# Kernel optimization log

Hardware: AMD Instinct MI355X
Metric: run time of the kernel (lower is better)

The kernel has to match this reference:

```python
import jax, jax.numpy as jnp
import numpy as np

B, S, D = 32, 2048, 64
SQRT_DIM = float(np.sqrt(D))  # scale=True -> divide by sqrt(dim)


def setup_inputs() -> dict:
    key = jax.random.key(0)
    kq, kk, kv, km = jax.random.split(key, 4)
    query = jax.random.normal(kq, (B, S, D), dtype=jnp.float32)
    key_t = jax.random.normal(kk, (B, S, D), dtype=jnp.float32)
    value = jax.random.normal(kv, (B, S, D), dtype=jnp.float32)
    mask = jax.random.randint(km, (B, S, S), 0, 2).astype(jnp.bool_)
    return {"query": query, "key": key_t, "value": value, "mask": mask}


def reference(query, key, value, mask):
    # score = Q @ K^T / sqrt(dim)   -> [B, S, S]
    score = jnp.einsum('bqd,bkd->bqk', query, key) / SQRT_DIM
    score = jnp.where(mask, jnp.float32(-1e9), score)  # masked_fill_
    attn = jax.nn.softmax(score, axis=-1)
    # context = attn @ V   -> [B, S, D]  (block_mask is None -> no gamma)
    context = jnp.einsum('bqk,bkd->bqd', attn, value)
    return (context, attn)
```

## Files before the change

kernel.cpp:

```cpp
#include <hip/hip_runtime.h>
#include <hip/hip_bf16.h>

#define BB 32
#define SS 2048
#define DD 64
#define NTH 256
#define QT 16
#define KTL 128
#define SCALE 0.125f

typedef __attribute__((ext_vector_type(4))) float f32x4;
typedef __attribute__((ext_vector_type(8))) short bf16x8;

union B8 { bf16x8 v; unsigned int u[4]; };

__device__ __forceinline__ unsigned int pk2bf(float a, float b) {
    __hip_bfloat162 h = __float22bfloat162_rn(make_float2(a, b));
    unsigned int u;
    __builtin_memcpy(&u, &h, 4);
    return u;
}
__device__ __forceinline__ float bf_lo(unsigned int w) {
    return __builtin_bit_cast(float, w << 16);
}
__device__ __forceinline__ float bf_hi(unsigned int w) {
    return __builtin_bit_cast(float, w & 0xffff0000u);
}

__global__ __launch_bounds__(NTH) void prepK(const float* __restrict__ K,
                                             unsigned short* __restrict__ Kbf) {
    const size_t i = (size_t)blockIdx.x * NTH + threadIdx.x;
    const float4* s = (const float4*)K;
    const float4 a = s[2 * i], c = s[2 * i + 1];
    uint4 w;
    w.x = pk2bf(a.x, a.y); w.y = pk2bf(a.z, a.w);
    w.z = pk2bf(c.x, c.y); w.w = pk2bf(c.z, c.w);
    ((uint4*)Kbf)[i] = w;
}

#define VPADF 68
__global__ __launch_bounds__(NTH) void prepV(const float* __restrict__ V,
                                             unsigned short* __restrict__ VTh,
                                             unsigned short* __restrict__ VTl) {
    __shared__ __align__(16) float lt[KTL * VPADF];
    const int t  = threadIdx.x;
    const int b  = blockIdx.x >> 4;
    const int ck = blockIdx.x & 15;
    const float4* Vs = (const float4*)(V + ((size_t)b * SS + ck * KTL) * DD);
    #pragma unroll
    for (int i = 0; i < 8; ++i) {
        const int f4 = i * NTH + t;
        float4 v = Vs[f4];
        const int kc = f4 >> 4, d4 = f4 & 15;
        *(float4*)&lt[kc * VPADF + d4 * 4] = v;
    }
    __syncthreads();
    const int d = t >> 2, kseg = t & 3;
    unsigned short* oh = VTh + ((size_t)b * DD + d) * SS + ck * KTL + kseg * 32;
    unsigned short* ol = VTl + ((size_t)b * DD + d) * SS + ck * KTL + kseg * 32;
    #pragma unroll
    for (int cch = 0; cch < 4; ++cch) {
        uint4 wh, wl;
        unsigned int* ph = (unsigned int*)&wh;
        unsigned int* pl = (unsigned int*)&wl;
        #pragma unroll
        for (int p = 0; p < 4; ++p) {
            const int k0 = kseg * 32 + cch * 8 + p * 2;
            const float a = lt[k0 * VPADF + d], c = lt[(k0 + 1) * VPADF + d];
            const unsigned int hw = pk2bf(a, c);
            ph[p] = hw;
            pl[p] = pk2bf(a - bf_lo(hw), c - bf_hi(hw));
        }
        *(uint4*)(oh + cch * 8) = wh;
        *(uint4*)(ol + cch * 8) = wl;
    }
}

__global__ __launch_bounds__(NTH, 4) void sdpa_mfma2(
    const float* __restrict__ Q, const int* __restrict__ M,
    const unsigned short* __restrict__ Kbf,
    const unsigned short* __restrict__ VTh, const unsigned short* __restrict__ VTl,
    float* __restrict__ ctx, float* __restrict__ attn)
{
    __shared__ __align__(16) unsigned char smem[17408];
    __shared__ float wsum[4][QT];
    __shared__ float inv_l[QT];
    unsigned short* bnc = (unsigned short*)smem;
    float*          scr = (float*)smem;

    const int t    = threadIdx.x;
    const int wave = t >> 6, l = t & 63, g = l >> 4, li = l & 15;
    const int b    = blockIdx.x >> 7;
    const int q0   = (blockIdx.x & 127) * QT;

    const unsigned short* Kb  = Kbf + (size_t)b * SS * DD;
    const unsigned short* Vhb = VTh + (size_t)b * DD * SS;
    const unsigned short* Vlb = VTl + (size_t)b * DD * SS;
    const int*   Mb   = M + ((size_t)b * SS + q0) * SS;
    float*       attb = attn + ((size_t)b * SS + q0) * SS;

    B8 qh[2], ql[2];
    {
        const float* qp = Q + ((size_t)(b * SS + q0 + li)) * DD + g * 8;
        #pragma unroll
        for (int h = 0; h < 2; ++h) {
            float f[8];
            *(float4*)&f[0] = *(const float4*)(qp + h * 32);
            *(float4*)&f[4] = *(const float4*)(qp + h * 32 + 4);
            #pragma unroll
            for (int i = 0; i < 4; ++i) {
                unsigned int hw = pk2bf(f[2*i], f[2*i+1]);
                qh[h].u[i] = hw;
                ql[h].u[i] = pk2bf(f[2*i] - bf_lo(hw), f[2*i+1] - bf_hi(hw));
            }
        }
    }

    const unsigned short* kf0 = Kb + (size_t)(wave * 32 + li) * DD + g * 8;

    auto qk = [&](int tl, f32x4& s0, f32x4& s1) {
        const unsigned short* p0 = kf0 + (size_t)tl * KTL * DD;
        #pragma unroll
        for (int h = 0; h < 2; ++h) {
            B8 k0, k1;
            k0.v = *(const bf16x8*)(p0 + 32 * h);
            k1.v = *(const bf16x8*)(p0 + 16 * DD + 32 * h);
            s0 = __builtin_amdgcn_mfma_f32_16x16x32_bf16(qh[h].v, k0.v, s0, 0, 0, 0);
            s0 = __builtin_amdgcn_mfma_f32_16x16x32_bf16(ql[h].v, k0.v, s0, 0, 0, 0);
            s1 = __builtin_amdgcn_mfma_f32_16x16x32_bf16(qh[h].v, k1.v, s1, 0, 0, 0);
            s1 = __builtin_amdgcn_mfma_f32_16x16x32_bf16(ql[h].v, k1.v, s1, 0, 0, 0);
        }
    };

    float lsum[4] = {0.f, 0.f, 0.f, 0.f};
    unsigned int mb0 = 0, mb1 = 0, mb2 = 0, mb3 = 0;

    #pragma unroll 1
    for (int tl = 0; tl < 16; ++tl) {
        const int kg0 = tl * KTL + wave * 32 + li;
        int m0a[4], m1a[4];
        #pragma unroll
        for (int r = 0; r < 4; ++r) {
            const size_t mo = (size_t)(g * 4 + r) * SS + kg0;
            m0a[r] = __builtin_nontemporal_load(&Mb[mo]);
            m1a[r] = __builtin_nontemporal_load(&Mb[mo + 16]);
        }
        f32x4 s0 = {0.f,0.f,0.f,0.f}, s1 = {0.f,0.f,0.f,0.f};
        qk(tl, s0, s1);
        unsigned int fl = 0;
        #pragma unroll
        for (int r = 0; r < 4; ++r) {
            float e0 = __expf(s0[r] * SCALE);
            float e1 = __expf(s1[r] * SCALE);
            if (m0a[r]) { fl |= 1u << r;       e0 = 0.f; }
            if (m1a[r]) { fl |= 1u << (4 + r); e1 = 0.f; }
            lsum[r] += e0 + e1;
        }
        mb0 = (mb0 >> 8) | (mb1 << 24);
        mb1 = (mb1 >> 8) | (mb2 << 24);
        mb2 = (mb2 >> 8) | (mb3 << 24);
        mb3 = (mb3 >> 8) | (fl << 24);
    }

    #pragma unroll
    for (int off = 8; off >= 1; off >>= 1)
        #pragma unroll
        for (int r = 0; r < 4; ++r)
            lsum[r] += __shfl_xor(lsum[r], off, 64);
    if (li == 0) {
        #pragma unroll
        for (int r = 0; r < 4; ++r) wsum[wave][g * 4 + r] = lsum[r];
    }
    __syncthreads();
    if (t < QT) inv_l[t] = 1.0f / (wsum[0][t] + wsum[1][t] + wsum[2][t] + wsum[3][t]);
    __syncthreads();
    float invl[4];
    #pragma unroll
    for (int r = 0; r < 4; ++r) invl[r] = inv_l[g * 4 + r];

    f32x4 cacc[4] = {{0.f,0.f,0.f,0.f},{0.f,0.f,0.f,0.f},{0.f,0.f,0.f,0.f},{0.f,0.f,0.f,0.f}};
    unsigned short* bw = bnc + wave * 512;

    #pragma unroll 1
    for (int tl = 0; tl < 16; ++tl) {
        f32x4 s0 = {0.f,0.f,0.f,0.f}, s1 = {0.f,0.f,0.f,0.f};
        qk(tl, s0, s1);
        const unsigned int fl = mb0 & 0xffu;
        mb0 = (mb0 >> 8) | (mb1 << 24);
        mb1 = (mb1 >> 8) | (mb2 << 24);
        mb2 = (mb2 >> 8) | (mb3 << 24);
        mb3 >>= 8;
        const int kg0 = tl * KTL + wave * 32 + li;
        #pragma unroll
        for (int r = 0; r < 4; ++r) {
            float e0 = ((fl >> r)       & 1u) ? 0.f : __expf(s0[r] * SCALE);
            float e1 = ((fl >> (4 + r)) & 1u) ? 0.f : __expf(s1[r] * SCALE);
            const size_t ao = (size_t)(g * 4 + r) * SS + kg0;
            attb[ao]      = e0 * invl[r];
            attb[ao + 16] = e1 * invl[r];
            const int q = g * 4 + r;
            const int b0 = li >> 3, b1 = (li + 16) >> 3;
            bw[((b0 * 16 + (q ^ b0)) << 3) + (li & 7)] = (unsigned short)pk2bf(e0, 0.f);
            bw[((b1 * 16 + (q ^ b1)) << 3) + (li & 7)] = (unsigned short)pk2bf(e1, 0.f);
        }
        B8 pf;
        pf.v = *(const bf16x8*)(bw + ((g * 16 + (li ^ g)) << 3));
        const size_t vcol = (size_t)tl * KTL + wave * 32 + g * 8;
        #pragma unroll
        for (int c = 0; c < 4; ++c) {
            const size_t voff = (size_t)(c * 16 + li) * SS + vcol;
            B8 vh, vl;
            vh.v = *(const bf16x8*)(Vhb + voff);
            vl.v = *(const bf16x8*)(Vlb + voff);
            cacc[c] = __builtin_amdgcn_mfma_f32_16x16x32_bf16(pf.v, vh.v, cacc[c], 0, 0, 0);
            cacc[c] = __builtin_amdgcn_mfma_f32_16x16x32_bf16(pf.v, vl.v, cacc[c], 0, 0, 0);
        }
    }

    __syncthreads();
    {
        const int row = wave * 64 + l;
        #pragma unroll
        for (int c = 0; c < 4; ++c)
            #pragma unroll
            for (int r = 0; r < 4; ++r)
                scr[row * 17 + c * 4 + r] = cacc[c][r];
    }
    __syncthreads();
    {
        const int q = t >> 4, d0 = (t & 15) * 4;
        float4 o;
        float* op = &o.x;
        #pragma unroll
        for (int dd = 0; dd < 4; ++dd) {
            const int d    = d0 + dd;
            const int lane = (q >> 2) * 16 + (d & 15);
            const int idx  = lane * 17 + (d >> 4) * 4 + (q & 3);
            float s = 0.f;
            #pragma unroll
            for (int w = 0; w < 4; ++w) s += scr[w * 64 * 17 + idx];
            op[dd] = s * inv_l[q];
        }
        *(float4*)(ctx + ((size_t)(b * SS + q0 + q)) * DD + d0) = o;
    }
}

extern "C" void kernel_launch(void* const* d_in, const int* in_sizes, int n_in,
                              void* d_out, int out_size, void* d_ws, size_t ws_size,
                              hipStream_t stream) {
    const float* Q = (const float*)d_in[0];
    const float* K = (const float*)d_in[1];
    const float* V = (const float*)d_in[2];
    const int*   M = (const int*)d_in[3];
    float* ctx  = (float*)d_out;
    float* attn = (float*)d_out + (size_t)BB * SS * DD;

    const size_t NE = (size_t)BB * SS * DD;
    unsigned short* Kbf = (unsigned short*)d_ws;
    unsigned short* VTh = Kbf + NE;
    unsigned short* VTl = VTh + NE;

    prepK<<<dim3((unsigned)(NE / 8 / NTH)), dim3(NTH), 0, stream>>>(K, Kbf);
    prepV<<<dim3(BB * (SS / KTL)), dim3(NTH), 0, stream>>>(V, VTh, VTl);
    sdpa_mfma2<<<dim3(BB * (SS / QT)), dim3(NTH), 0, stream>>>(Q, M, Kbf, VTh, VTl, ctx, attn);
}
```

Measured before the change: 1.287 ms.

## Prepack mask into bitmasks in separate kernel, raise occupancy, swizzle block order

Adds a packM kernel that compresses each row's int32 mask into per-lane 32-bit bitmasks, so the attention kernel loads four words per thread instead of streaming int mask values inside its first pass. The first pass drops the mask loads and the shift-register bookkeeping. It also raises launch bounds to 8 blocks per CU and swizzles the block index so neighbouring blocks spread across batches. The mask is still read in full once, but by a separate pass with an extra launch and workspace, and the higher occupancy target may force register spills.

```diff
diff --git a/kernel.cpp b/kernel.cpp
--- a/kernel.cpp
+++ b/kernel.cpp
@@ -76,8 +76,25 @@
     }
 }
 
-__global__ __launch_bounds__(NTH, 4) void sdpa_mfma2(
-    const float* __restrict__ Q, const int* __restrict__ M,
+__global__ __launch_bounds__(NTH) void packM(const int* __restrict__ M,
+                                             unsigned int* __restrict__ Mp) {
+    const int t = threadIdx.x, w = t >> 6, l = t & 63;
+    const size_t row = (size_t)blockIdx.x * 4 + w;
+    const int* mr = M + row * SS;
+    const int kb = (l >> 4) * 32 + (l & 15);
+    unsigned int bits = 0;
+    #pragma unroll
+    for (int tl = 0; tl < 16; ++tl) {
+        const int m0 = __builtin_nontemporal_load(&mr[tl * 128 + kb]);
+        const int m1 = __builtin_nontemporal_load(&mr[tl * 128 + kb + 16]);
+        bits |= (m0 ? 1u : 0u) << (2 * tl);
+        bits |= (m1 ? 1u : 0u) << (2 * tl + 1);
+    }
+    Mp[row * 64 + l] = bits;
+}
+
+__global__ __launch_bounds__(NTH, 8) void sdpa_mfma2(
+    const float* __restrict__ Q, const unsigned int* __restrict__ Mp,
     const unsigned short* __restrict__ Kbf,
     const unsigned short* __restrict__ VTh, const unsigned short* __restrict__ VTl,
     float* __restrict__ ctx, float* __restrict__ attn)
@@ -90,14 +107,22 @@
 
     const int t    = threadIdx.x;
     const int wave = t >> 6, l = t & 63, g = l >> 4, li = l & 15;
-    const int b    = blockIdx.x >> 7;
-    const int q0   = (blockIdx.x & 127) * QT;
+    const unsigned int bid = blockIdx.x;
+    const unsigned int swz = (bid & 7) * 512 + (bid >> 3);
+    const int b    = swz >> 7;
+    const int q0   = (swz & 127) * QT;
 
     const unsigned short* Kb  = Kbf + (size_t)b * SS * DD;
     const unsigned short* Vhb = VTh + (size_t)b * DD * SS;
     const unsigned short* Vlb = VTl + (size_t)b * DD * SS;
-    const int*   Mb   = M + ((size_t)b * SS + q0) * SS;
-    float*       attb = attn + ((size_t)b * SS + q0) * SS;
+    float* attb = attn + ((size_t)b * SS + q0) * SS;
+
+    unsigned int mreg[4];
+    {
+        const unsigned int* Mpb = Mp + ((size_t)b * SS + q0) * 64 + (wave * 16 + li);
+        #pragma unroll
+        for (int r = 0; r < 4; ++r) mreg[r] = Mpb[(size_t)(g * 4 + r) * 64];
+    }
 
     B8 qh[2], ql[2];
     {
@@ -133,68 +158,47 @@
     };
 
     float lsum[4] = {0.f, 0.f, 0.f, 0.f};
-    unsigned int mb0 = 0, mb1 = 0, mb2 = 0, mb3 = 0;
-
-    #pragma unroll 1
-    for (int tl = 0; tl < 16; ++tl) {
-        const int kg0 = tl * KTL + wave * 32 + li;
-        int m0a[4], m1a[4];
-        #pragma unroll
-        for (int r = 0; r < 4; ++r) {
-            const size_t mo = (size_t)(g * 4 + r) * SS + kg0;
-            m0a[r] = __builtin_nontemporal_load(&Mb[mo]);
-            m1a[r] = __builtin_nontemporal_load(&Mb[mo + 16]);
-        }
-        f32x4 s0 = {0.f,0.f,0.f,0.f}, s1 = {0.f,0.f,0.f,0.f};
-        qk(tl, s0, s1);
-        unsigned int fl = 0;
-        #pragma unroll
-        for (int r = 0; r < 4; ++r) {
-            float e0 = __expf(s0[r] * SCALE);
-            float e1 = __expf(s1[r] * SCALE);
-            if (m0a[r]) { fl |= 1u << r;       e0 = 0.f; }
-            if (m1a[r]) { fl |= 1u << (4 + r); e1 = 0.f; }
-            lsum[r] += e0 + e1;
-        }
-        mb0 = (mb0 >> 8) | (mb1 << 24);
-        mb1 = (mb1 >> 8) | (mb2 << 24);
-        mb2 = (mb2 >> 8) | (mb3 << 24);
-        mb3 = (mb3 >> 8) | (fl << 24);
-    }
-
-    #pragma unroll
-    for (int off = 8; off >= 1; off >>= 1)
-        #pragma unroll
-        for (int r = 0; r < 4; ++r)
-            lsum[r] += __shfl_xor(lsum[r], off, 64);
-    if (li == 0) {
-        #pragma unroll
-        for (int r = 0; r < 4; ++r) wsum[wave][g * 4 + r] = lsum[r];
-    }
-    __syncthreads();
-    if (t < QT) inv_l[t] = 1.0f / (wsum[0][t] + wsum[1][t] + wsum[2][t] + wsum[3][t]);
-    __syncthreads();
-    float invl[4];
-    #pragma unroll
-    for (int r = 0; r < 4; ++r) invl[r] = inv_l[g * 4 + r];
-
-    f32x4 cacc[4] = {{0.f,0.f,0.f,0.f},{0.f,0.f,0.f,0.f},{0.f,0.f,0.f,0.f},{0.f,0.f,0.f,0.f}};
-    unsigned short* bw = bnc + wave * 512;
 
     #pragma unroll 1
     for (int tl = 0; tl < 16; ++tl) {
         f32x4 s0 = {0.f,0.f,0.f,0.f}, s1 = {0.f,0.f,0.f,0.f};
         qk(tl, s0, s1);
-        const unsigned int fl = mb0 & 0xffu;
-        mb0 = (mb0 >> 8) | (mb1 << 24);
-        mb1 = (mb1 >> 8) | (mb2 << 24);
-        mb2 = (mb2 >> 8) | (mb3 << 24);
-        mb3 >>= 8;
+        #pragma unroll
+        for (int r = 0; r < 4; ++r) {
+            const float e0 = ((mreg[r] >> (2 * tl))     & 1u) ? 0.f : __expf(s0[r] * SCALE);
+            const float e1 = ((mreg[r] >> (2 * tl + 1)) & 1u) ? 0.f : __expf(s1[r] * SCALE);
+            lsum[r] += e0 + e1;
+        }
+    }
+
+    #pragma unroll
+    for (int off = 8; off >= 1; off >>= 1)
+        #pragma unroll
+        for (int r = 0; r < 4; ++r)
+            lsum[r] += __shfl_xor(lsum[r], off, 64);
+    if (li == 0) {
+        #pragma unroll
+        for (int r = 0; r < 4; ++r) wsum[wave][g * 4 + r] = lsum[r];
+    }
+    __syncthreads();
+    if (t < QT) inv_l[t] = 1.0f / (wsum[0][t] + wsum[1][t] + wsum[2][t] + wsum[3][t]);
+    __syncthreads();
+    float invl[4];
+    #pragma unroll
+    for (int r = 0; r < 4; ++r) invl[r] = inv_l[g * 4 + r];
+
+    f32x4 cacc[4] = {{0.f,0.f,0.f,0.f},{0.f,0.f,0.f,0.f},{0.f,0.f,0.f,0.f},{0.f,0.f,0.f,0.f}};
+    unsigned short* bw = bnc + wave * 512;
+
+    #pragma unroll 1
+    for (int tl = 0; tl < 16; ++tl) {
+        f32x4 s0 = {0.f,0.f,0.f,0.f}, s1 = {0.f,0.f,0.f,0.f};
+        qk(tl, s0, s1);
         const int kg0 = tl * KTL + wave * 32 + li;
         #pragma unroll
         for (int r = 0; r < 4; ++r) {
-            float e0 = ((fl >> r)       & 1u) ? 0.f : __expf(s0[r] * SCALE);
-            float e1 = ((fl >> (4 + r)) & 1u) ? 0.f : __expf(s1[r] * SCALE);
+            const float e0 = ((mreg[r] >> (2 * tl))     & 1u) ? 0.f : __expf(s0[r] * SCALE);
+            const float e1 = ((mreg[r] >> (2 * tl + 1)) & 1u) ? 0.f : __expf(s1[r] * SCALE);
             const size_t ao = (size_t)(g * 4 + r) * SS + kg0;
             attb[ao]      = e0 * invl[r];
             attb[ao + 16] = e1 * invl[r];
@@ -259,8 +263,10 @@
     unsigned short* Kbf = (unsigned short*)d_ws;
     unsigned short* VTh = Kbf + NE;
     unsigned short* VTl = VTh + NE;
+    unsigned int*   Mpk = (unsigned int*)(VTl + NE);
 
     prepK<<<dim3((unsigned)(NE / 8 / NTH)), dim3(NTH), 0, stream>>>(K, Kbf);
     prepV<<<dim3(BB * (SS / KTL)), dim3(NTH), 0, stream>>>(V, VTh, VTl);
-    sdpa_mfma2<<<dim3(BB * (SS / QT)), dim3(NTH), 0, stream>>>(Q, M, Kbf, VTh, VTl, ctx, attn);
-}
+    packM<<<dim3(BB * SS / 4), dim3(NTH), 0, stream>>>(M, Mpk);
+    sdpa_mfma2<<<dim3(BB * (SS / QT)), dim3(NTH), 0, stream>>>(Q, Mpk, Kbf, VTh, VTl, ctx, attn);
+}
```

New measurement: 1.386 ms. 7.7% more time.
